# Kernel optimization log

Measured on AMD Instinct MI355X. Metric: run time of the kernel, lower is better.

## Reference

```python
import jax, jax.numpy as jnp
import numpy as np

B, CIN, COUT = 4, 256, 256
H, W = 48, 48
KH = KW = 7
SH = SW = 1
PH = PW = 3
REL = COUT // 2  # rel_size with groups=1


def setup_inputs() -> dict:
    key = jax.random.key(0)
    ks = jax.random.split(key, 7)
    fan = float(CIN)
    x = jax.random.normal(ks[0], (B, CIN, H, W), jnp.float32)
    w_q = jax.random.normal(ks[1], (COUT, CIN), jnp.float32) * (2.0 / fan) ** 0.5
    w_k = jax.random.normal(ks[2], (COUT, CIN), jnp.float32) * (2.0 / fan) ** 0.5
    w_v = jax.random.normal(ks[3], (COUT, CIN), jnp.float32) * (2.0 / fan) ** 0.5
    bound = 1.0 / np.sqrt(COUT)
    bias = jax.random.uniform(ks[4], (1, COUT, 1, 1), jnp.float32, -bound, bound)
    rel_x = jax.random.normal(ks[5], (REL, KW), jnp.float32)
    rel_y = jax.random.normal(ks[6], (COUT - REL, KH), jnp.float32)
    return {"x": x, "w_q": w_q, "w_k": w_k, "w_v": w_v, "bias": bias,
            "rel_x": rel_x, "rel_y": rel_y}


def reference(x, w_q, w_k, w_v, bias, rel_x, rel_y):
    b = x.shape[0]
    ph, pw = H + 2 * PH, W + 2 * PW
    fh = (ph - KH) // SH + 1
    fw = (pw - KW) // SW + 1
    xp = jnp.pad(x, ((0, 0), (0, 0), (PH, PH), (PW, PW)))
    # 1x1 convs (groups=1) as channel matmuls
    vq = jnp.einsum('oc,bchw->bohw', w_q, xp)
    vk = jnp.einsum('oc,bchw->bohw', w_k, xp)
    vv = jnp.einsum('oc,bchw->bohw', w_v, xp)
    # query at window centers: [b, C, fh, fw]
    win_q = vq[:, :, (KH - 1) // 2: ph - KH // 2: SH, (KW - 1) // 2: pw - KW // 2: SW]
    # relative position terms (sum over channel halves)
    qx = jnp.einsum('bxhw,xk->bhwk', win_q[:, :REL], rel_x)        # [b,fh,fw,kw]
    qy = jnp.einsum('byhw,yk->bhwk', win_q[:, REL:], rel_y)        # [b,fh,fw,kh]
    # overlapping windows via gather (equivalent to torch unfold)
    I = jnp.arange(fh)[:, None] * SH + jnp.arange(KH)[None, :]     # [fh,kh]
    J = jnp.arange(fw)[:, None] * SW + jnp.arange(KW)[None, :]     # [fw,kw]
    win_k = vk[:, :, I[:, None, :, None], J[None, :, None, :]]     # [b,C,fh,fw,kh,kw]
    # channel-summed attention logits (shared across channels, as in source)
    scores = jnp.einsum('bchw,bchwkl->bhwkl', win_q, win_k)
    scores = scores + qy[:, :, :, :, None] + qx[:, :, :, None, :]
    attn = jax.nn.softmax(scores.reshape(b, fh, fw, KH * KW), axis=-1)
    attn = attn.reshape(b, fh, fw, KH, KW)
    win_v = vv[:, :, I[:, None, :, None], J[None, :, None, :]]     # [b,C,fh,fw,kh,kw]
    out = jnp.einsum('bhwkl,bchwkl->bchw', attn, win_v) + bias
    return out
```

## Files before the change

kernel.cpp:

```cpp
#include <hip/hip_runtime.h>

#define BB 4
#define CC 256
#define HH 48
#define WW 48
#define HWHW 2304
#define KK 49
#define RELN 128

#define QSZ (BB*CC*HWHW)
#define ATTNOFF (3*QSZ)
#define SBUF_FLOATS (BB*HH*64*WW)
#define WTOFF (ATTNOFF + SBUF_FLOATS)
#define WT_FLOATS 196608
#define KBOFF (WTOFF + WT_FLOATS)
#define KB_FLOATS 3145728
#define RBOFF (KBOFF + KB_FLOATS)

typedef short bf16x8 __attribute__((ext_vector_type(8)));
typedef float f32x4 __attribute__((ext_vector_type(4)));

__device__ __forceinline__ void split_bf16(float f, unsigned short& hi, unsigned short& lo)
{
    unsigned u = __float_as_uint(f);
    hi = (unsigned short)(u >> 16);
    float r = f - __uint_as_float(u & 0xFFFF0000u);
    unsigned v = __float_as_uint(r);
    v += 0x7FFFu + ((v >> 16) & 1u);
    lo = (unsigned short)(v >> 16);
}

__device__ __forceinline__ void gload16(const uint4* g, uint4* l)
{
    __builtin_amdgcn_global_load_lds(
        (const __attribute__((address_space(1))) void*)g,
        (__attribute__((address_space(3))) void*)l, 16, 0, 0);
}

__global__ __launch_bounds__(256) void prep_kernel(
    const float* __restrict__ x,
    const float* __restrict__ wq, const float* __restrict__ wk,
    const float* __restrict__ wvp,
    const float* __restrict__ relx, const float* __restrict__ rely,
    unsigned short* __restrict__ xt, unsigned short* __restrict__ wt,
    float* __restrict__ ws)
{
    __shared__ unsigned short lds[32*520];
    const int bid = blockIdx.x;
    const int t = threadIdx.x;

    if (bid < 288) {
        const int b = bid / 72;
        const int hw0 = (bid % 72) * 32;
        const int hw = t & 31, cp = t >> 5;
        #pragma unroll 4
        for (int i = 0; i < 32; ++i) {
            int c = i*8 + cp;
            float f = x[((size_t)b*CC + c)*HWHW + hw0 + hw];
            unsigned short hi, lo; split_bf16(f, hi, lo);
            int ch = i*2;
            lds[hw*520 + ((ch       ^ (hw&7))*8) + cp] = hi;
            lds[hw*520 + (((ch + 1) ^ (hw&7))*8) + cp] = lo;
        }
        __syncthreads();
        const int hw2 = t >> 3, u = t & 7;
        uint4* xt4 = (uint4*)xt;
        const size_t rowbase = ((size_t)b*HWHW + hw0 + hw2) * 64;
        #pragma unroll
        for (int j = 0; j < 8; ++j) {
            int chunk = j*8 + u;
            uint4 v = *(const uint4*)&lds[hw2*520 + chunk*8];
            xt4[rowbase + chunk] = v;
        }
        return;
    }
    if (bid < 384) {
        const int tt = (bid - 288)*256 + t;
        const int m = tt >> 5, kg = tt & 31;
        const float* src = (m < 256) ? wq : (m < 512) ? wk : wvp;
        const float* row = src + (size_t)(m & 255)*256 + kg*8;
        unsigned short h[8], l[8];
        #pragma unroll
        for (int j = 0; j < 8; ++j) split_bf16(row[j], h[j], l[j]);
        uint4 hv, lv;
        hv.x = (unsigned)h[0] | ((unsigned)h[1]<<16); hv.y = (unsigned)h[2] | ((unsigned)h[3]<<16);
        hv.z = (unsigned)h[4] | ((unsigned)h[5]<<16); hv.w = (unsigned)h[6] | ((unsigned)h[7]<<16);
        lv.x = (unsigned)l[0] | ((unsigned)l[1]<<16); lv.y = (unsigned)l[2] | ((unsigned)l[3]<<16);
        lv.z = (unsigned)l[4] | ((unsigned)l[5]<<16); lv.w = (unsigned)l[6] | ((unsigned)l[7]<<16);
        uint4* dstrow = (uint4*)wt + (size_t)m*64;
        const int ks = kg >> 2, s_hi = 2*(kg & 3);
        dstrow[ks*8 + ( s_hi      ^ (m&7))] = hv;
        dstrow[ks*8 + ((s_hi + 1) ^ (m&7))] = lv;
        return;
    }
    if (bid < 576) {
        uint4* kb4 = (uint4*)(ws + KBOFF);
        const uint4 z = make_uint4(0u,0u,0u,0u);
        int u0 = (bid - 384)*256 + t;
        #pragma unroll
        for (int it = 0; it < 4; ++it) {
            int u = u0 + it*49152;
            int bch = u >> 7, rem = u & 127;
            int r16 = rem >> 3, gr = rem & 7;
            int r = (r16 < 3) ? r16 : 48 + r16;
            kb4[((size_t)bch*64 + r)*8 + gr] = z;
        }
        return;
    }
    {
        unsigned short* rb = (unsigned short*)(ws + RBOFF);
        #pragma unroll
        for (int it = 0; it < 4; ++it) {
            int idx = t + it*256;
            int gi  = idx & 7;
            int l   = (idx >> 3) & 15;
            int ck4 = (idx >> 7) & 3;
            int rel = idx >> 9;
            int isLo = gi >> 2, g4i = gi & 3;
            unsigned short vals[8];
            #pragma unroll
            for (int j = 0; j < 8; ++j) {
                int cl = ck4*32 + g4i*8 + j;
                float f = (l < 7) ? (rel ? rely[cl*7 + l] : relx[cl*7 + l]) : 0.f;
                unsigned short hi, lo; split_bf16(f, hi, lo);
                vals[j] = isLo ? lo : hi;
            }
            int slot = gi ^ (l & 7);
            unsigned short* dst = rb + (((size_t)rel*4 + ck4)*16 + l)*64 + slot*8;
            uint4 pack;
            pack.x = (unsigned)vals[0] | ((unsigned)vals[1]<<16);
            pack.y = (unsigned)vals[2] | ((unsigned)vals[3]<<16);
            pack.z = (unsigned)vals[4] | ((unsigned)vals[5]<<16);
            pack.w = (unsigned)vals[6] | ((unsigned)vals[7]<<16);
            *(uint4*)dst = pack;
        }
    }
}

__global__ __launch_bounds__(512) void proj_gemm_kernel(
    const unsigned short* __restrict__ xt,
    const unsigned short* __restrict__ wt,
    float* __restrict__ ws)
{
    __shared__ uint4 smem[2][2560];
    const int m0 = blockIdx.x * 256;
    const int n0 = blockIdx.y * 64;
    const int b = n0 / HWHW;
    const int hwb = n0 % HWHW;
    const int tid = threadIdx.x;
    const int wid = tid >> 6, ln = tid & 63;
    const int wm = wid >> 1, wn = wid & 1;
    const int l15 = ln & 15, g = ln >> 4;

    f32x4 acc[4][2];
    #pragma unroll
    for (int i = 0; i < 4; ++i)
        #pragma unroll
        for (int j = 0; j < 2; ++j) acc[i][j] = (f32x4){0.f,0.f,0.f,0.f};

    const uint4* wt4 = (const uint4*)wt;
    const uint4* xt4 = (const uint4*)xt;
    const int lrow = ln >> 3, lslot = ln & 7;

    #define STAGE(bf, ks)                                                          \
        {                                                                          \
            _Pragma("unroll")                                                      \
            for (int i = 0; i < 4; ++i) {                                          \
                int seg = wid*4 + i;                                               \
                int row = seg*8 + lrow;                                            \
                gload16(wt4 + (size_t)(m0 + row)*64 + (ks)*8 + lslot,              \
                        &smem[bf][seg*64]);                                        \
            }                                                                      \
            {                                                                      \
                int row = wid*8 + lrow;                                            \
                gload16(xt4 + (size_t)(n0 + row)*64 + (ks)*8 + lslot,              \
                        &smem[bf][2048 + wid*64]);                                 \
            }                                                                      \
        }

    STAGE(0, 0);
    #pragma unroll
    for (int ks = 0; ks < 8; ++ks) {
        const int cur = ks & 1;
        if (ks < 7) STAGE(cur ^ 1, ks + 1);
        if (ks < 7) asm volatile("s_waitcnt vmcnt(5)" ::: "memory");
        else        asm volatile("s_waitcnt vmcnt(0)" ::: "memory");
        __builtin_amdgcn_s_barrier();
        __builtin_amdgcn_sched_barrier(0);
        bf16x8 aH[4], aL[4], bH[2], bL[2];
        #pragma unroll
        for (int mt = 0; mt < 4; ++mt) {
            int rA = wm*64 + mt*16 + l15;
            aH[mt] = *(const bf16x8*)&smem[cur][rA*8 + ((2*g)   ^ (rA&7))];
            aL[mt] = *(const bf16x8*)&smem[cur][rA*8 + ((2*g+1) ^ (rA&7))];
        }
        #pragma unroll
        for (int nt = 0; nt < 2; ++nt) {
            int rB = wn*32 + nt*16 + l15;
            bH[nt] = *(const bf16x8*)&smem[cur][2048 + rB*8 + ((2*g)   ^ (rB&7))];
            bL[nt] = *(const bf16x8*)&smem[cur][2048 + rB*8 + ((2*g+1) ^ (rB&7))];
        }
        #pragma unroll
        for (int mt = 0; mt < 4; ++mt)
            #pragma unroll
            for (int nt = 0; nt < 2; ++nt) {
                acc[mt][nt] = __builtin_amdgcn_mfma_f32_16x16x32_bf16(aH[mt], bH[nt], acc[mt][nt], 0, 0, 0);
                acc[mt][nt] = __builtin_amdgcn_mfma_f32_16x16x32_bf16(aH[mt], bL[nt], acc[mt][nt], 0, 0, 0);
                acc[mt][nt] = __builtin_amdgcn_mfma_f32_16x16x32_bf16(aL[mt], bH[nt], acc[mt][nt], 0, 0, 0);
            }
        if (ks < 7) {
            asm volatile("s_waitcnt lgkmcnt(0)" ::: "memory");
            __builtin_amdgcn_s_barrier();
        }
    }
    #undef STAGE

    const int proj = blockIdx.x;
    if (proj == 2) {
        #pragma unroll
        for (int mt = 0; mt < 4; ++mt) {
            int ch4 = wm*16 + mt*4 + g;
            #pragma unroll
            for (int nt = 0; nt < 2; ++nt) {
                int hw = hwb + wn*32 + nt*16 + l15;
                float* dst = ws + (size_t)2*QSZ + (((size_t)b*64 + ch4)*HWHW + hw)*4;
                *(f32x4*)dst = acc[mt][nt];
            }
        }
        return;
    }
    __syncthreads();
    unsigned short* eb = (unsigned short*)&smem[0][0];
    #pragma unroll
    for (int mt = 0; mt < 4; ++mt) {
        const int chb = wm*64 + mt*16 + 4*g;
        const int ck = chb >> 5;
        const int p = chb & 31, g8 = p >> 3, half = (p >> 2) & 1;
        #pragma unroll
        for (int nt = 0; nt < 2; ++nt) {
            const int hwl = wn*32 + nt*16 + l15;
            const int w = (hwb + hwl) % 48;
            const int key = (proj == 0 ? w : w + 3) & 7;
            f32x4 v = acc[mt][nt];
            unsigned short h0,h1,h2,h3,q0,q1,q2,q3;
            split_bf16(v[0],h0,q0); split_bf16(v[1],h1,q1);
            split_bf16(v[2],h2,q2); split_bf16(v[3],h3,q3);
            uint2 hv, lv;
            hv.x = (unsigned)h0 | ((unsigned)h1<<16); hv.y = (unsigned)h2 | ((unsigned)h3<<16);
            lv.x = (unsigned)q0 | ((unsigned)q1<<16); lv.y = (unsigned)q2 | ((unsigned)q3<<16);
            const int base = (ck*64 + hwl)*64;
            *(uint2*)(eb + base + ((g8 ^ key)*8 + half*4))     = hv;
            *(uint2*)(eb + base + (((g8+4) ^ key)*8 + half*4)) = lv;
        }
    }
    __syncthreads();
    if (proj == 0) {
        const uint4* src = (const uint4*)eb;
        uint4* qb4 = (uint4*)ws;
        #pragma unroll
        for (int ck = 0; ck < 8; ++ck) {
            uint4* dst = qb4 + (((size_t)b*8 + ck)*HWHW + hwb)*8;
            dst[tid] = src[ck*512 + tid];
        }
    } else {
        uint4* kb4 = (uint4*)(ws + KBOFF);
        const uint4* src = (const uint4*)eb;
        #pragma unroll
        for (int it = 0; it < 8; ++it) {
            int u = it*512 + tid;
            int row = u >> 3, gr = u & 7;
            int ck = row >> 6, hwl = row & 63;
            int hw2 = hwb + hwl, h2 = hw2/48, w2 = hw2%48;
            kb4[((((size_t)b*8 + ck)*48 + h2)*64 + (w2+3))*8 + gr] = src[u];
        }
    }
}

__global__ __launch_bounds__(512) void scores2_kernel(float* __restrict__ ws)
{
    __shared__ unsigned short sAll[2][4096*8];
    __shared__ float sc[63][48];

    const int bid = blockIdx.x;
    const int b = bid / 48, h = bid % 48;
    const int tid = threadIdx.x;
    const int wv = tid >> 6, ln = tid & 63;
    const int l15 = ln & 15, g4 = ln >> 4;
    const int key = l15 & 7;

    const unsigned short* QB = (const unsigned short*)ws;
    const unsigned short* KB = (const unsigned short*)(ws + KBOFF);
    const unsigned short* RB = (const unsigned short*)(ws + RBOFF);

    for (int u = tid; u < 63*48; u += 512) ((float*)sc)[u] = 0.f;

    const int dk = wv;
    const int hp = h + dk - 3;
    const bool dok = (wv < 7) && (hp >= 0) && (hp < 48);

    f32x4 acc[6], qx[3], qy[3];
    #pragma unroll
    for (int i = 0; i < 6; ++i) acc[i] = (f32x4){0.f,0.f,0.f,0.f};
    #pragma unroll
    for (int i = 0; i < 3; ++i) { qx[i] = (f32x4){0.f,0.f,0.f,0.f}; qy[i] = (f32x4){0.f,0.f,0.f,0.f}; }

    #define SSTAGE(bf, ck)                                                         \
        {                                                                          \
            _Pragma("unroll")                                                      \
            for (int e = 0; e < 8; ++e) {                                          \
                const int I = wv*8 + e;                                            \
                uint4* dst = (uint4*)sAll[bf] + I*64;                              \
                if (I < 6) {                                                       \
                    int unit = I*64 + ln; int row = unit >> 3, gr = unit & 7;      \
                    gload16((const uint4*)QB                                       \
                        + ((((size_t)b*8 + (ck))*48 + h)*48 + row)*8 + gr, dst);   \
                } else if (I < 62) {                                               \
                    int uk = (I-6)*64 + ln;                                        \
                    int kri = uk >> 9;                                             \
                    int wi = uk & 511; int row = wi >> 3, gr = wi & 7;             \
                    int kh = h + kri - 3;                                          \
                    int khc = kh < 0 ? 0 : (kh > 47 ? 47 : kh);                    \
                    gload16((const uint4*)KB                                       \
                        + ((((size_t)b*8 + (ck))*48 + khc)*64 + row)*8 + gr, dst); \
                } else {                                                           \
                    int ur = (I-62)*64 + ln; int row = ur >> 3, gr = ur & 7;       \
                    int rel = (ck) >> 2, c4 = (ck) & 3;                            \
                    gload16((const uint4*)RB                                       \
                        + (((size_t)rel*4 + c4)*16 + row)*8 + gr, dst);            \
                }                                                                  \
            }                                                                      \
        }

    SSTAGE(0, 0);
    for (int ck = 0; ck < 8; ++ck) {
        const int cur = ck & 1;
        if (ck < 7) SSTAGE(cur ^ 1, ck + 1);
        if (ck < 7) asm volatile("s_waitcnt vmcnt(8)" ::: "memory");
        else        asm volatile("s_waitcnt vmcnt(0)" ::: "memory");
        __builtin_amdgcn_s_barrier();
        __builtin_amdgcn_sched_barrier(0);

        const unsigned short* sQ = sAll[cur];
        const unsigned short* sK = sAll[cur] + 384*8;
        const unsigned short* sR = sAll[cur] + 3968*8;

        bf16x8 AH[3], AL[3];
        #pragma unroll
        for (int i = 0; i < 3; ++i) {
            const unsigned short* qr = sQ + (16*i + l15)*64;
            AH[i] = *(const bf16x8*)(qr + ((g4       ^ key)*8));
            AL[i] = *(const bf16x8*)(qr + (((g4 + 4) ^ key)*8));
        }

        if (wv < 7) {
            if (dok) {
                const unsigned short* kbase = sK + dk*4096;
                bf16x8 BH[4], BL[4];
                #pragma unroll
                for (int j = 0; j < 4; ++j) {
                    const unsigned short* kr = kbase + (j*16 + l15)*64;
                    BH[j] = *(const bf16x8*)(kr + ((g4       ^ key)*8));
                    BL[j] = *(const bf16x8*)(kr + (((g4 + 4) ^ key)*8));
                }
                #pragma unroll
                for (int i = 0; i < 3; ++i) {
                    acc[i*2]   = __builtin_amdgcn_mfma_f32_16x16x32_bf16(AH[i], BH[i],   acc[i*2],   0,0,0);
                    acc[i*2]   = __builtin_amdgcn_mfma_f32_16x16x32_bf16(AH[i], BL[i],   acc[i*2],   0,0,0);
                    acc[i*2]   = __builtin_amdgcn_mfma_f32_16x16x32_bf16(AL[i], BH[i],   acc[i*2],   0,0,0);
                    acc[i*2+1] = __builtin_amdgcn_mfma_f32_16x16x32_bf16(AH[i], BH[i+1], acc[i*2+1], 0,0,0);
                    acc[i*2+1] = __builtin_amdgcn_mfma_f32_16x16x32_bf16(AH[i], BL[i+1], acc[i*2+1], 0,0,0);
                    acc[i*2+1] = __builtin_amdgcn_mfma_f32_16x16x32_bf16(AL[i], BH[i+1], acc[i*2+1], 0,0,0);
                }
            }
        } else {
            const unsigned short* rr = sR + l15*64;
            bf16x8 RH = *(const bf16x8*)(rr + ((g4       ^ key)*8));
            bf16x8 RL = *(const bf16x8*)(rr + (((g4 + 4) ^ key)*8));
            if (ck < 4) {
                #pragma unroll
                for (int i = 0; i < 3; ++i) {
                    qx[i] = __builtin_amdgcn_mfma_f32_16x16x32_bf16(AH[i], RH, qx[i], 0,0,0);
                    qx[i] = __builtin_amdgcn_mfma_f32_16x16x32_bf16(AH[i], RL, qx[i], 0,0,0);
                    qx[i] = __builtin_amdgcn_mfma_f32_16x16x32_bf16(AL[i], RH, qx[i], 0,0,0);
                }
            } else {
                #pragma unroll
                for (int i = 0; i < 3; ++i) {
                    qy[i] = __builtin_amdgcn_mfma_f32_16x16x32_bf16(AH[i], RH, qy[i], 0,0,0);
                    qy[i] = __builtin_amdgcn_mfma_f32_16x16x32_bf16(AH[i], RL, qy[i], 0,0,0);
                    qy[i] = __builtin_amdgcn_mfma_f32_16x16x32_bf16(AL[i], RH, qy[i], 0,0,0);
                }
            }
        }
        if (ck < 7) {
            asm volatile("s_waitcnt lgkmcnt(0)" ::: "memory");
            __builtin_amdgcn_s_barrier();
        }
    }
    #undef SSTAGE

    const int n = l15;
    if (wv < 7) {
        if (dok) {
            #pragma unroll
            for (int i = 0; i < 3; ++i)
                #pragma unroll
                for (int a = 0; a < 2; ++a) {
                    f32x4 A = acc[i*2+a];
                    #pragma unroll
                    for (int r = 0; r < 4; ++r) {
                        int m = 4*g4 + r;
                        int dl = n - m + a*16;
                        if (dl >= 0 && dl < 7)
                            sc[dk*7 + dl][16*i + m] = A[r];
                    }
                }
        }
    } else {
        if (n < 7) {
            #pragma unroll
            for (int i = 0; i < 3; ++i)
                #pragma unroll
                for (int r = 0; r < 4; ++r) {
                    sc[49 + n][16*i + 4*g4 + r] = qx[i][r];
                    sc[56 + n][16*i + 4*g4 + r] = qy[i][r];
                }
        }
    }
    __syncthreads();

    if (tid < 48) {
        const int w = tid;
        float tot[KK], rx[7], ry[7];
        #pragma unroll
        for (int i = 0; i < KK; ++i) tot[i] = sc[i][w];
        #pragma unroll
        for (int l = 0; l < 7; ++l) { rx[l] = sc[49+l][w]; ry[l] = sc[56+l][w]; }
        float mx = -1e30f;
        #pragma unroll
        for (int dk2 = 0; dk2 < 7; ++dk2)
            #pragma unroll
            for (int dl = 0; dl < 7; ++dl) {
                tot[dk2*7+dl] += ry[dk2] + rx[dl];
                mx = fmaxf(mx, tot[dk2*7+dl]);
            }
        float sum = 0.f;
        #pragma unroll
        for (int i = 0; i < KK; ++i) { float e = __expf(tot[i]-mx); tot[i]=e; sum += e; }
        float inv = 1.f/sum;
        float* base = ws + ATTNOFF + ((size_t)(b*HH + h)*64)*WW + w;
        #pragma unroll
        for (int i = 0; i < KK; ++i) base[(size_t)i*WW] = tot[i]*inv;
    }
}

__global__ __launch_bounds__(128) void pv_kernel(
    const float* __restrict__ bias,
    const float* __restrict__ ws,
    float* __restrict__ out)
{
    const float* vbuf = ws + (size_t)2*QSZ;
    const float* attn = ws + ATTNOFF;

    const int bid = blockIdx.x;
    const int pxt = bid % 18;
    const int pgq = (bid / 18) % 16;
    const int b   = bid / (18*16);

    const int tid = threadIdx.x;
    const int pxg = tid & 31;
    const int pg  = pgq*4 + (tid >> 5);

    const int hw0 = pxt*128 + pxg*4;
    const int w0 = hw0 % WW;
    const int h0 = hw0 / WW;

    const float* vb = vbuf + ((size_t)b*64 + pg)*HWHW*4;
    const float* ab = attn + ((size_t)(b*HH + h0)*64)*WW;

    const float4 b4 = *(const float4*)(bias + pg*4);
    f32x4 bias4 = (f32x4){b4.x, b4.y, b4.z, b4.w};
    f32x4 acc[4];
    #pragma unroll
    for (int p = 0; p < 4; ++p) acc[p] = bias4;

    #pragma unroll
    for (int dk = 0; dk < 7; ++dk) {
        const int gr = h0 + dk - 3;
        const bool rok = (gr >= 0 && gr < HH);
        f32x4 vrow[10];
        #pragma unroll
        for (int jj = 0; jj < 10; ++jj) {
            const int gc = w0 - 3 + jj;
            vrow[jj] = (rok && gc >= 0 && gc < WW)
                ? *(const f32x4*)(vb + ((size_t)gr*WW + gc)*4)
                : (f32x4){0.f,0.f,0.f,0.f};
        }
        const float* arow = ab + (size_t)(dk*7)*WW + w0;
        #pragma unroll
        for (int dl = 0; dl < 7; ++dl) {
            const float4 av = *(const float4*)(arow + (size_t)dl*WW);
            acc[0] += vrow[dl+0] * av.x;
            acc[1] += vrow[dl+1] * av.y;
            acc[2] += vrow[dl+2] * av.z;
            acc[3] += vrow[dl+3] * av.w;
        }
    }
    #pragma unroll
    for (int c = 0; c < 4; ++c) {
        float4 o;
        o.x = acc[0][c]; o.y = acc[1][c]; o.z = acc[2][c]; o.w = acc[3][c];
        *(float4*)(out + ((size_t)b*CC + pg*4 + c)*HWHW + hw0) = o;
    }
}

extern "C" void kernel_launch(void* const* d_in, const int* in_sizes, int n_in,
                              void* d_out, int out_size, void* d_ws, size_t ws_size,
                              hipStream_t stream) {
    const float* x    = (const float*)d_in[0];
    const float* wq   = (const float*)d_in[1];
    const float* wk   = (const float*)d_in[2];
    const float* wv   = (const float*)d_in[3];
    const float* bias = (const float*)d_in[4];
    const float* relx = (const float*)d_in[5];
    const float* rely = (const float*)d_in[6];
    float* ws  = (float*)d_ws;
    float* out = (float*)d_out;
    unsigned short* xt = (unsigned short*)d_out;
    unsigned short* wt = (unsigned short*)(ws + WTOFF);

    prep_kernel<<<dim3(577), dim3(256), 0, stream>>>(x, wq, wk, wv, relx, rely, xt, wt, ws);
    proj_gemm_kernel<<<dim3(3, 144), dim3(512), 0, stream>>>(xt, wt, ws);
    scores2_kernel<<<dim3(BB*HH), dim3(512), 0, stream>>>(ws);
    pv_kernel<<<dim3(BB*16*18), dim3(128), 0, stream>>>(bias, ws, out);
}
```

Baseline: 72.43 us.

## Stage V tile in shared memory and keep attention weights in registers in pv_kernel

Restructures the attention-times-V kernel so each block handles 4 output rows by 16 channels. The halo'd V tile is loaded cooperatively into LDS and each thread holds its 49 attention weights in registers, reused across 4 channel quads. Each thread now owns one pixel instead of 4 pixels by 4 channels. This is meant to cut redundant global V loads and repeated attention reads, at the cost of about 36KB of LDS per block, a barrier, higher register pressure, and scalar rather than float4 output stores.

```diff
diff --git a/kernel.cpp b/kernel.cpp
--- a/kernel.cpp
+++ b/kernel.cpp
@@ -454,63 +454,56 @@
     }
 }
 
-__global__ __launch_bounds__(128) void pv_kernel(
+__global__ __launch_bounds__(192) void pv_kernel(
     const float* __restrict__ bias,
     const float* __restrict__ ws,
     float* __restrict__ out)
 {
     const float* vbuf = ws + (size_t)2*QSZ;
     const float* attn = ws + ATTNOFF;
+    __shared__ f32x4 vtile[4*10*56];
 
     const int bid = blockIdx.x;
-    const int pxt = bid % 18;
-    const int pgq = (bid / 18) % 16;
-    const int b   = bid / (18*16);
-
-    const int tid = threadIdx.x;
-    const int pxg = tid & 31;
-    const int pg  = pgq*4 + (tid >> 5);
-
-    const int hw0 = pxt*128 + pxg*4;
-    const int w0 = hw0 % WW;
-    const int h0 = hw0 / WW;
-
-    const float* vb = vbuf + ((size_t)b*64 + pg)*HWHW*4;
-    const float* ab = attn + ((size_t)(b*HH + h0)*64)*WW;
-
-    const float4 b4 = *(const float4*)(bias + pg*4);
-    f32x4 bias4 = (f32x4){b4.x, b4.y, b4.z, b4.w};
-    f32x4 acc[4];
-    #pragma unroll
-    for (int p = 0; p < 4; ++p) acc[p] = bias4;
-
-    #pragma unroll
-    for (int dk = 0; dk < 7; ++dk) {
-        const int gr = h0 + dk - 3;
-        const bool rok = (gr >= 0 && gr < HH);
-        f32x4 vrow[10];
-        #pragma unroll
-        for (int jj = 0; jj < 10; ++jj) {
-            const int gc = w0 - 3 + jj;
-            vrow[jj] = (rok && gc >= 0 && gc < WW)
-                ? *(const f32x4*)(vb + ((size_t)gr*WW + gc)*4)
-                : (f32x4){0.f,0.f,0.f,0.f};
-        }
-        const float* arow = ab + (size_t)(dk*7)*WW + w0;
-        #pragma unroll
-        for (int dl = 0; dl < 7; ++dl) {
-            const float4 av = *(const float4*)(arow + (size_t)dl*WW);
-            acc[0] += vrow[dl+0] * av.x;
-            acc[1] += vrow[dl+1] * av.y;
-            acc[2] += vrow[dl+2] * av.z;
-            acc[3] += vrow[dl+3] * av.w;
-        }
-    }
-    #pragma unroll
-    for (int c = 0; c < 4; ++c) {
-        float4 o;
-        o.x = acc[0][c]; o.y = acc[1][c]; o.z = acc[2][c]; o.w = acc[3][c];
-        *(float4*)(out + ((size_t)b*CC + pg*4 + c)*HWHW + hw0) = o;
+    const int cg = bid & 15;
+    const int hs = (bid >> 4) % 12;
+    const int b  = bid / (16*12);
+    const int h0 = hs*4;
+
+    const int t = threadIdx.x;
+    const int hl = t / 48, w = t % 48;
+    const int h = h0 + hl;
+
+    const float* ab = attn + ((size_t)(b*HH + h)*64)*WW + w;
+    float a[KK];
+    #pragma unroll
+    for (int i = 0; i < KK; ++i) a[i] = ab[(size_t)i*WW];
+
+    for (int s = t; s < 4*10*56; s += 192) {
+        int chq = s / 560;
+        int rem = s - chq*560;
+        int row = rem / 56, wslot = rem - row*56;
+        int gr = h0 + row - 3, gc = wslot - 3;
+        f32x4 v = (f32x4){0.f,0.f,0.f,0.f};
+        if (gr >= 0 && gr < HH && gc >= 0 && gc < WW)
+            v = *(const f32x4*)(vbuf + (((size_t)b*64 + cg*4 + chq)*HWHW + gr*WW + gc)*4);
+        vtile[s] = v;
+    }
+    __syncthreads();
+
+    #pragma unroll
+    for (int chq = 0; chq < 4; ++chq) {
+        const float4 b4 = *(const float4*)(bias + cg*16 + chq*4);
+        f32x4 acc = (f32x4){b4.x, b4.y, b4.z, b4.w};
+        #pragma unroll
+        for (int dk = 0; dk < 7; ++dk) {
+            const f32x4* vrow = &vtile[(chq*10 + hl + dk)*56 + w];
+            #pragma unroll
+            for (int dl = 0; dl < 7; ++dl)
+                acc += vrow[dl] * a[dk*7+dl];
+        }
+        float* ob = out + ((size_t)(b*CC + cg*16 + chq*4))*HWHW + (size_t)h*WW + w;
+        #pragma unroll
+        for (int c = 0; c < 4; ++c) ob[(size_t)c*HWHW] = acc[c];
     }
 }
 
@@ -532,5 +525,5 @@
     prep_kernel<<<dim3(577), dim3(256), 0, stream>>>(x, wq, wk, wv, relx, rely, xt, wt, ws);
     proj_gemm_kernel<<<dim3(3, 144), dim3(512), 0, stream>>>(xt, wt, ws);
     scores2_kernel<<<dim3(BB*HH), dim3(512), 0, stream>>>(ws);
-    pv_kernel<<<dim3(BB*16*18), dim3(128), 0, stream>>>(bias, ws, out);
-}
+    pv_kernel<<<dim3(BB*12*16), dim3(192), 0, stream>>>(bias, ws, out);
+}
```

After: 64.52 us, median of 2. -10.9%, faster.
